# Optimization experiments

Hardware: AMD Instinct MI355X
Metric: run time of the kernel (lower is better)

## Reference

```python
import jax, jax.numpy as jnp
import numpy as np

PH, PW = 16, 16  # patch_size


def setup_inputs() -> dict:
    key = jax.random.key(0)
    k1, k2, k3 = jax.random.split(key, 3)
    B, C, H, W = 32, 3, 512, 512
    N, D = 196, 768
    x = jax.random.normal(k1, (B, C, H, W), dtype=jnp.float32)
    centers = jax.random.randint(k2, (B, N, 2), 0, 512, dtype=jnp.int32)
    Wp = jax.random.normal(k3, (PH * PW * C, D), dtype=jnp.float32) * 0.02
    bp = jnp.zeros((D,), dtype=jnp.float32)
    return {"x": x, "centers": centers, "W": Wp, "b": bp}


def reference(x, centers, W, b):
    # x: [B,C,H,Wd], centers: [B,N,2] (h,w), W: [PH*PW*C, D], b: [D]
    B, C, H, Wd = x.shape
    N = centers.shape[1]
    # start indices clipped to valid range (original zero-pads OOB patches;
    # here we clamp so every center yields one in-bounds patch, fixed count)
    sh = jnp.clip(centers[..., 0] - PH // 2, 0, H - PH)
    sw = jnp.clip(centers[..., 1] - PW // 2, 0, Wd - PW)

    def slice_one(img, h0, w0):
        return jax.lax.dynamic_slice(img, (0, h0, w0), (C, PH, PW))

    per_image = jax.vmap(slice_one, in_axes=(None, 0, 0))   # over N patches
    extract = jax.vmap(per_image, in_axes=(0, 0, 0))        # over batch
    patches = extract(x, sh, sw)                             # [B,N,C,PH,PW]
    flat = patches.reshape(B, N, C * PH * PW)                # flatten(start_dim=1) per patch
    return flat @ W + b                                      # [B,N,D]
```

## Files before the change

kernel.cpp:

```cpp
#include <hip/hip_runtime.h>
#include <hip/hip_bf16.h>
#include <stdint.h>

#define PHh 16
#define PWw 16
#define Bn  32
#define Cn  3
#define Hn  512
#define Wn  512
#define Nn  196
#define Dn  768
#define Kn  768
#define Mn  (Bn * Nn)

typedef __attribute__((ext_vector_type(8))) short   short8;
typedef __attribute__((ext_vector_type(4))) float   f32x4;

__global__ void gather_patches(const float* __restrict__ x,
                               const int* __restrict__ centers,
                               __hip_bfloat16* __restrict__ A) {
    int idx = blockIdx.x * blockDim.x + threadIdx.x;
    const int total8 = Mn * Kn / 8;
    if (idx >= total8) return;
    int e = idx * 8;
    int m = e / Kn;
    int k = e - m * Kn;
    int b = m / Nn;
    int ch = centers[m * 2 + 0];
    int cw = centers[m * 2 + 1];
    int sh = min(max(ch - PHh / 2, 0), Hn - PHh);
    int sw = min(max(cw - PWw / 2, 0), Wn - PWw);
    int c  = k >> 8;
    int r  = k & 255;
    int ph = r >> 4;
    int pw = r & 15;
    const float* src = x + ((size_t)(b * Cn + c) * Hn + (sh + ph)) * Wn + (sw + pw);
    float4 lo = *reinterpret_cast<const float4*>(src);
    float4 hi = *reinterpret_cast<const float4*>(src + 4);
    __hip_bfloat16 v[8];
    v[0] = __float2bfloat16(lo.x); v[1] = __float2bfloat16(lo.y);
    v[2] = __float2bfloat16(lo.z); v[3] = __float2bfloat16(lo.w);
    v[4] = __float2bfloat16(hi.x); v[5] = __float2bfloat16(hi.y);
    v[6] = __float2bfloat16(hi.z); v[7] = __float2bfloat16(hi.w);
    *reinterpret_cast<short8*>(A + e) = *reinterpret_cast<const short8*>(v);
}

__global__ void transpose_w(const float* __restrict__ W,
                            __hip_bfloat16* __restrict__ Wt) {
    __shared__ float tile[32][33];
    int d0 = blockIdx.x * 32;
    int k0 = blockIdx.y * 32;
    int lx = threadIdx.x & 31;
    int ly = threadIdx.x >> 5;
#pragma unroll
    for (int i = 0; i < 4; ++i) {
        int kk = ly + i * 8;
        tile[kk][lx] = W[(size_t)(k0 + kk) * Dn + d0 + lx];
    }
    __syncthreads();
#pragma unroll
    for (int i = 0; i < 4; ++i) {
        int dd = ly + i * 8;
        Wt[(size_t)(d0 + dd) * Kn + k0 + lx] = __float2bfloat16(tile[lx][dd]);
    }
}

__device__ __forceinline__ void gload_lds16(const __hip_bfloat16* g,
                                            __hip_bfloat16* l) {
    __builtin_amdgcn_global_load_lds(
        (const __attribute__((address_space(1))) void*)g,
        (__attribute__((address_space(3))) void*)l, 16, 0, 0);
}

__global__ __launch_bounds__(256, 4) void gemm_bt(
    const __hip_bfloat16* __restrict__ A,
    const __hip_bfloat16* __restrict__ Bt,
    const float* __restrict__ bias,
    float* __restrict__ C) {
    __shared__ __hip_bfloat16 As[64 * 32];
    __shared__ __hip_bfloat16 Bs[128 * 32];

    const int bm = blockIdx.x;
    const int bn = blockIdx.y;
    const int tid = threadIdx.x;
    const int w = tid >> 6;
    const int l = tid & 63;
    const int wr = w >> 1;
    const int wc = w & 1;

    const int srow = w * 16 + (l >> 2);
    const int skk  = (l & 3) * 8;
    const __hip_bfloat16* Ag = A  + (size_t)(bm * 64  + srow) * Kn + skk;
    const __hip_bfloat16* Bg = Bt + (size_t)(bn * 128 + srow) * Kn + skk;

    const int fr = l & 15;
    const int fq = l >> 4;

    f32x4 acc[2][4] = {};

    for (int t = 0; t < Kn / 32; ++t) {
        gload_lds16(Ag,           As + w * 512);
        gload_lds16(Bg,           Bs + w * 512);
        gload_lds16(Bg + 64 * Kn, Bs + 2048 + w * 512);
        Ag += 32; Bg += 32;
        __syncthreads();

        short8 af[2], bfrag[4];
#pragma unroll
        for (int m = 0; m < 2; ++m)
            af[m] = *reinterpret_cast<const short8*>(
                &As[(wr * 32 + m * 16 + fr) * 32 + fq * 8]);
#pragma unroll
        for (int n = 0; n < 4; ++n)
            bfrag[n] = *reinterpret_cast<const short8*>(
                &Bs[(wc * 64 + n * 16 + fr) * 32 + fq * 8]);
#pragma unroll
        for (int m = 0; m < 2; ++m)
#pragma unroll
            for (int n = 0; n < 4; ++n)
                acc[m][n] = __builtin_amdgcn_mfma_f32_16x16x32_bf16(
                    af[m], bfrag[n], acc[m][n], 0, 0, 0);
        __syncthreads();
    }

#pragma unroll
    for (int n = 0; n < 4; ++n) {
        int col = bn * 128 + wc * 64 + n * 16 + fr;
        float bv = bias[col];
#pragma unroll
        for (int m = 0; m < 2; ++m) {
            int row0 = bm * 64 + wr * 32 + m * 16 + fq * 4;
#pragma unroll
            for (int j = 0; j < 4; ++j)
                C[(size_t)(row0 + j) * Dn + col] = acc[m][n][j] + bv;
        }
    }
}

__global__ void naive_patch_embed(const float* __restrict__ x,
                                  const int* __restrict__ centers,
                                  const float* __restrict__ W,
                                  const float* __restrict__ bias,
                                  float* __restrict__ out) {
    int idx = blockIdx.x * blockDim.x + threadIdx.x;
    if (idx >= Mn * Dn) return;
    int m = idx / Dn;
    int d = idx - m * Dn;
    int b = m / Nn;
    int ch = centers[m * 2 + 0];
    int cw = centers[m * 2 + 1];
    int sh = min(max(ch - 8, 0), Hn - PHh);
    int sw = min(max(cw - 8, 0), Wn - PWw);
    float accv = bias[d];
    for (int c = 0; c < Cn; ++c)
        for (int ph = 0; ph < PHh; ++ph) {
            const float* row = x + ((size_t)(b * Cn + c) * Hn + sh + ph) * Wn + sw;
            const float* wr = W + (size_t)(c * 256 + ph * 16) * Dn + d;
#pragma unroll
            for (int pw = 0; pw < PWw; ++pw)
                accv += row[pw] * wr[(size_t)pw * Dn];
        }
    out[idx] = accv;
}

extern "C" void kernel_launch(void* const* d_in, const int* in_sizes, int n_in,
                              void* d_out, int out_size, void* d_ws, size_t ws_size,
                              hipStream_t stream) {
    const float* x       = (const float*)d_in[0];
    const int*   centers = (const int*)d_in[1];
    const float* W       = (const float*)d_in[2];
    const float* bias    = (const float*)d_in[3];
    float*       out     = (float*)d_out;

    const size_t needA = (size_t)Mn * Kn * sizeof(__hip_bfloat16);
    const size_t needW = (size_t)Kn * Dn * sizeof(__hip_bfloat16);

    if (ws_size >= needA + needW) {
        __hip_bfloat16* Abf = (__hip_bfloat16*)d_ws;
        __hip_bfloat16* Wt  = (__hip_bfloat16*)((char*)d_ws + needA);

        int g1 = (Mn * Kn / 8 + 255) / 256;
        gather_patches<<<g1, 256, 0, stream>>>(x, centers, Abf);

        dim3 g2(Dn / 32, Kn / 32);
        transpose_w<<<g2, 256, 0, stream>>>(W, Wt);

        dim3 g3(Mn / 64, Dn / 128);
        gemm_bt<<<g3, 256, 0, stream>>>(Abf, Wt, bias, out);
    } else {
        int g = (Mn * Dn + 255) / 256;
        naive_patch_embed<<<g, 256, 0, stream>>>(x, centers, W, bias, out);
    }
}
```

Before: 166.0 us.

## Fuse patch gather and bf16 conversion into the GEMM A-tile load

Removes the separate gather kernel and its bf16 intermediate buffer. The GEMM now reads fp32 pixels for its A tile directly from the image at the clamped patch offsets, converts them to bf16 in registers, and stores them into LDS. The next k-slice is prefetched into registers before the barrier so the load overlaps compute. This saves the write and re-read of the patch matrix and one launch, but the image gets read again by each of the 6 column blocks through cache, and A loads now go through registers instead of direct-to-LDS.

```diff
diff --git a/kernel.cpp b/kernel.cpp
--- a/kernel.cpp
+++ b/kernel.cpp
@@ -15,35 +15,6 @@
 
 typedef __attribute__((ext_vector_type(8))) short   short8;
 typedef __attribute__((ext_vector_type(4))) float   f32x4;
-
-__global__ void gather_patches(const float* __restrict__ x,
-                               const int* __restrict__ centers,
-                               __hip_bfloat16* __restrict__ A) {
-    int idx = blockIdx.x * blockDim.x + threadIdx.x;
-    const int total8 = Mn * Kn / 8;
-    if (idx >= total8) return;
-    int e = idx * 8;
-    int m = e / Kn;
-    int k = e - m * Kn;
-    int b = m / Nn;
-    int ch = centers[m * 2 + 0];
-    int cw = centers[m * 2 + 1];
-    int sh = min(max(ch - PHh / 2, 0), Hn - PHh);
-    int sw = min(max(cw - PWw / 2, 0), Wn - PWw);
-    int c  = k >> 8;
-    int r  = k & 255;
-    int ph = r >> 4;
-    int pw = r & 15;
-    const float* src = x + ((size_t)(b * Cn + c) * Hn + (sh + ph)) * Wn + (sw + pw);
-    float4 lo = *reinterpret_cast<const float4*>(src);
-    float4 hi = *reinterpret_cast<const float4*>(src + 4);
-    __hip_bfloat16 v[8];
-    v[0] = __float2bfloat16(lo.x); v[1] = __float2bfloat16(lo.y);
-    v[2] = __float2bfloat16(lo.z); v[3] = __float2bfloat16(lo.w);
-    v[4] = __float2bfloat16(hi.x); v[5] = __float2bfloat16(hi.y);
-    v[6] = __float2bfloat16(hi.z); v[7] = __float2bfloat16(hi.w);
-    *reinterpret_cast<short8*>(A + e) = *reinterpret_cast<const short8*>(v);
-}
 
 __global__ void transpose_w(const float* __restrict__ W,
                             __hip_bfloat16* __restrict__ Wt) {
@@ -72,8 +43,9 @@
         (__attribute__((address_space(3))) void*)l, 16, 0, 0);
 }
 
-__global__ __launch_bounds__(256, 4) void gemm_bt(
-    const __hip_bfloat16* __restrict__ A,
+__global__ __launch_bounds__(256, 4) void fused_patch_gemm(
+    const float* __restrict__ x,
+    const int* __restrict__ centers,
     const __hip_bfloat16* __restrict__ Bt,
     const float* __restrict__ bias,
     float* __restrict__ C) {
@@ -88,9 +60,18 @@
     const int wr = w >> 1;
     const int wc = w & 1;
 
+    const int ml = tid >> 2;
+    const int q  = tid & 3;
+    const int m  = bm * 64 + ml;
+    const int b  = m / Nn;
+    const int2 cc = *reinterpret_cast<const int2*>(centers + 2 * m);
+    const int sh = min(max(cc.x - PHh / 2, 0), Hn - PHh);
+    const int sw = min(max(cc.y - PWw / 2, 0), Wn - PWw);
+    const float* xbase = x + ((size_t)(b * Cn) * Hn + sh) * Wn + sw;
+    __hip_bfloat16* adst = As + tid * 8;
+
     const int srow = w * 16 + (l >> 2);
     const int skk  = (l & 3) * 8;
-    const __hip_bfloat16* Ag = A  + (size_t)(bm * 64  + srow) * Kn + skk;
     const __hip_bfloat16* Bg = Bt + (size_t)(bn * 128 + srow) * Kn + skk;
 
     const int fr = l & 15;
@@ -98,29 +79,54 @@
 
     f32x4 acc[2][4] = {};
 
+    auto srcAt = [&](int t) -> const float* {
+        int k0 = t * 32 + q * 8;
+        int c  = k0 >> 8;
+        int ph = (k0 >> 4) & 15;
+        int pw = k0 & 15;
+        return xbase + ((size_t)c * Hn + ph) * Wn + pw;
+    };
+
+    const float* s0 = srcAt(0);
+    float4 lo = *reinterpret_cast<const float4*>(s0);
+    float4 hi = *reinterpret_cast<const float4*>(s0 + 4);
+
     for (int t = 0; t < Kn / 32; ++t) {
-        gload_lds16(Ag,           As + w * 512);
         gload_lds16(Bg,           Bs + w * 512);
         gload_lds16(Bg + 64 * Kn, Bs + 2048 + w * 512);
-        Ag += 32; Bg += 32;
+        Bg += 32;
+
+        __hip_bfloat16 v[8];
+        v[0] = __float2bfloat16(lo.x); v[1] = __float2bfloat16(lo.y);
+        v[2] = __float2bfloat16(lo.z); v[3] = __float2bfloat16(lo.w);
+        v[4] = __float2bfloat16(hi.x); v[5] = __float2bfloat16(hi.y);
+        v[6] = __float2bfloat16(hi.z); v[7] = __float2bfloat16(hi.w);
+        *reinterpret_cast<short8*>(adst) = *reinterpret_cast<const short8*>(v);
+
+        const float* sn = srcAt(t < Kn / 32 - 1 ? t + 1 : 0);
+        float4 nlo = *reinterpret_cast<const float4*>(sn);
+        float4 nhi = *reinterpret_cast<const float4*>(sn + 4);
+
         __syncthreads();
 
         short8 af[2], bfrag[4];
 #pragma unroll
-        for (int m = 0; m < 2; ++m)
-            af[m] = *reinterpret_cast<const short8*>(
-                &As[(wr * 32 + m * 16 + fr) * 32 + fq * 8]);
+        for (int mm = 0; mm < 2; ++mm)
+            af[mm] = *reinterpret_cast<const short8*>(
+                &As[(wr * 32 + mm * 16 + fr) * 32 + fq * 8]);
 #pragma unroll
         for (int n = 0; n < 4; ++n)
             bfrag[n] = *reinterpret_cast<const short8*>(
                 &Bs[(wc * 64 + n * 16 + fr) * 32 + fq * 8]);
 #pragma unroll
-        for (int m = 0; m < 2; ++m)
+        for (int mm = 0; mm < 2; ++mm)
 #pragma unroll
             for (int n = 0; n < 4; ++n)
-                acc[m][n] = __builtin_amdgcn_mfma_f32_16x16x32_bf16(
-                    af[m], bfrag[n], acc[m][n], 0, 0, 0);
+                acc[mm][n] = __builtin_amdgcn_mfma_f32_16x16x32_bf16(
+                    af[mm], bfrag[n], acc[mm][n], 0, 0, 0);
         __syncthreads();
+
+        lo = nlo; hi = nhi;
     }
 
 #pragma unroll
@@ -128,11 +134,11 @@
         int col = bn * 128 + wc * 64 + n * 16 + fr;
         float bv = bias[col];
 #pragma unroll
-        for (int m = 0; m < 2; ++m) {
-            int row0 = bm * 64 + wr * 32 + m * 16 + fq * 4;
+        for (int mm = 0; mm < 2; ++mm) {
+            int row0 = bm * 64 + wr * 32 + mm * 16 + fq * 4;
 #pragma unroll
             for (int j = 0; j < 4; ++j)
-                C[(size_t)(row0 + j) * Dn + col] = acc[m][n][j] + bv;
+                C[(size_t)(row0 + j) * Dn + col] = acc[mm][n][j] + bv;
         }
     }
 }
@@ -172,21 +178,16 @@
     const float* bias    = (const float*)d_in[3];
     float*       out     = (float*)d_out;
 
-    const size_t needA = (size_t)Mn * Kn * sizeof(__hip_bfloat16);
     const size_t needW = (size_t)Kn * Dn * sizeof(__hip_bfloat16);
 
-    if (ws_size >= needA + needW) {
-        __hip_bfloat16* Abf = (__hip_bfloat16*)d_ws;
-        __hip_bfloat16* Wt  = (__hip_bfloat16*)((char*)d_ws + needA);
-
-        int g1 = (Mn * Kn / 8 + 255) / 256;
-        gather_patches<<<g1, 256, 0, stream>>>(x, centers, Abf);
+    if (ws_size >= needW) {
+        __hip_bfloat16* Wt = (__hip_bfloat16*)d_ws;
 
         dim3 g2(Dn / 32, Kn / 32);
         transpose_w<<<g2, 256, 0, stream>>>(W, Wt);
 
         dim3 g3(Mn / 64, Dn / 128);
-        gemm_bt<<<g3, 256, 0, stream>>>(Abf, Wt, bias, out);
+        fused_patch_gemm<<<g3, 256, 0, stream>>>(x, centers, Wt, bias, out);
     } else {
         int g = (Mn * Dn + 255) / 256;
         naive_patch_embed<<<g, 256, 0, stream>>>(x, centers, W, bias, out);
```

New measurement: 165.9 us, median of 2. No clear change (-0.1%).
